# Kernel optimization log

Measured on AMD Instinct MI355X. Metric: run time of the kernel, lower is better.

## Reference

```python
import jax, jax.numpy as jnp
import numpy as np

N_PER_G = 6            # EEG channels per graph (complete graph incl. self-loops)
ALPHA = 0.5
BETA1 = float(np.log(1.0 / 1 + 1.0))  # GCN2Conv layer=1, lambda=1
BETA2 = float(np.log(1.0 / 2 + 1.0))  # GCN2Conv layer=2
BN_EPS = 1e-5


def setup_inputs() -> dict:
    key = jax.random.key(0)
    ks = jax.random.split(key, 10)
    G = 400_000
    N = G * N_PER_G          # 2.4M nodes
    E = G * N_PER_G * N_PER_G  # 14.4M edges (complete graph per EEG window)

    x = jax.random.normal(ks[0], (N, 6), dtype=jnp.float32)
    edge_weights = jax.random.uniform(ks[1], (E,), dtype=jnp.float32)

    # Batched complete-graph connectivity (numpy, structured)
    base = (np.arange(G, dtype=np.int64) * N_PER_G)
    ls = np.repeat(np.arange(N_PER_G), N_PER_G)   # local src
    ld = np.tile(np.arange(N_PER_G), N_PER_G)     # local dst
    src = jnp.asarray((base[:, None] + ls[None, :]).reshape(-1).astype(np.int32))
    dst = jnp.asarray((base[:, None] + ld[None, :]).reshape(-1).astype(np.int32))

    s6 = 1.0 / np.sqrt(6.0)
    W1 = jax.random.normal(ks[2], (6, 6), dtype=jnp.float32) * s6
    b1 = jnp.zeros((6,), dtype=jnp.float32)
    W2 = jax.random.normal(ks[3], (6, 6), dtype=jnp.float32) * s6
    b2 = jnp.zeros((6,), dtype=jnp.float32)
    gamma = jnp.ones((6,), dtype=jnp.float32)
    beta_bn = jnp.zeros((6,), dtype=jnp.float32)
    fcW1 = jax.random.normal(ks[4], (6, 10), dtype=jnp.float32) * s6   # xavier-ish
    fcb1 = jnp.zeros((10,), dtype=jnp.float32)
    fcW2 = jax.random.normal(ks[5], (10, 2), dtype=jnp.float32) * (1.0 / np.sqrt(10.0))
    fcb2 = jnp.zeros((2,), dtype=jnp.float32)

    return {"x": x, "edge_weights": edge_weights, "W1": W1, "b1": b1,
            "W2": W2, "b2": b2, "gamma": gamma, "beta_bn": beta_bn,
            "fcW1": fcW1, "fcb1": fcb1, "fcW2": fcW2, "fcb2": fcb2,
            "src": src, "dst": dst, "num_graphs": G}


def _gcn2_conv(feat, feat0, W, b, beta, edge_weights, src, dst, norm, n_nodes):
    # DGL GCN2Conv: sym-norm edge-weighted aggregation, identity mixing, proj mixing
    h = feat * norm                                   # [N,6]
    msg = h[src] * edge_weights[:, None]              # [E,6] gather
    agg = jax.ops.segment_sum(msg, dst, num_segments=n_nodes)  # [N,6] scatter-add
    h = agg * norm
    h = (1.0 - ALPHA) * h + ALPHA * feat0
    return (1.0 - beta) * h + beta * (h @ W) + b


def reference(x, edge_weights, W1, b1, W2, b2, gamma, beta_bn,
              fcW1, fcb1, fcW2, fcb2, src, dst, num_graphs):
    N = x.shape[0]
    # symmetric normalization from in-degrees (clamped to 1)
    deg = jax.ops.segment_sum(jnp.ones_like(edge_weights), dst, num_segments=N)
    norm = jax.lax.rsqrt(jnp.maximum(deg, 1.0))[:, None]  # [N,1]

    h = jax.nn.leaky_relu(_gcn2_conv(x, x, W1, b1, BETA1, edge_weights, src, dst, norm, N))
    h = _gcn2_conv(h, h, W2, b2, BETA2, edge_weights, src, dst, norm, N)

    # BatchNorm1d over nodes (training-mode batch statistics)
    mean = jnp.mean(h, axis=0)
    var = jnp.mean(jnp.square(h - mean), axis=0)
    h = (h - mean) * jax.lax.rsqrt(var + BN_EPS) * gamma + beta_bn
    h = jax.nn.leaky_relu(h)

    # SumPooling per graph (node i belongs to graph i // 6)
    gid = jnp.arange(N, dtype=jnp.int32) // N_PER_G
    pooled = jax.ops.segment_sum(h, gid, num_segments=num_graphs)  # [G,6]

    out = jax.nn.leaky_relu(pooled @ fcW1 + fcb1)  # dropout is identity at inference
    out = out @ fcW2 + fcb2                        # [G,2]
    return out
```

## Files before the change

### kernel.cpp

```cpp
#include <hip/hip_runtime.h>
#include <cstddef>
#include <cstdint>

#define NSLOT 64
#define ALPHA 0.5f
#define B1f   0.6931471805599453f
#define B2f   0.4054651081081644f

__device__ __forceinline__ float lrelu(float v) { return v >= 0.0f ? v : 0.01f * v; }

__device__ __forceinline__ float gc(const float4* a, int idx) {
  const float4 v = a[idx >> 2];
  const int c = idx & 3;
  return c == 0 ? v.x : (c == 1 ? v.y : (c == 2 ? v.z : v.w));
}

__device__ __forceinline__ unsigned pkbf(float a, float b) {
  unsigned ua = __float_as_uint(a), ub = __float_as_uint(b);
  ua += 0x7FFFu + ((ua >> 16) & 1u);
  ub += 0x7FFFu + ((ub >> 16) & 1u);
  return (ua >> 16) | (ub & 0xFFFF0000u);
}

__device__ __forceinline__ void gl_lds16(const float4* gp, float4* lbase, int lane) {
#if __has_builtin(__builtin_amdgcn_global_load_lds)
  __builtin_amdgcn_global_load_lds(
      (const __attribute__((address_space(1))) void*)(const void*)gp,
      (__attribute__((address_space(3))) void*)(void*)lbase, 16, 0, 0);
#else
  lbase[lane] = *gp;
#endif
}

__device__ __forceinline__ void compute_h2(const float4* X, const float4* Wt,
                                           const float* __restrict__ gW1,
                                           const float* __restrict__ gb1,
                                           const float* __restrict__ gW2,
                                           const float* __restrict__ gb2,
                                           float h2[36]) {
  float t[36];
#pragma unroll
  for (int j = 0; j < 6; ++j)
#pragma unroll
    for (int f = 0; f < 6; ++f) {
      float a = 0.f;
#pragma unroll
      for (int i = 0; i < 6; ++i) a = fmaf(gc(Wt, i * 6 + j), gc(X, i * 6 + f), a);
      t[j * 6 + f] = fmaf(a, ALPHA * (1.f / 6.f), ALPHA * gc(X, j * 6 + f));
    }
  float h1[36];
#pragma unroll
  for (int j = 0; j < 6; ++j)
#pragma unroll
    for (int f = 0; f < 6; ++f) {
      float a = 0.f;
#pragma unroll
      for (int k = 0; k < 6; ++k) a = fmaf(t[j * 6 + k], gW1[k * 6 + f], a);
      h1[j * 6 + f] = lrelu(fmaf(B1f, a, fmaf(1.f - B1f, t[j * 6 + f], gb1[f])));
    }
#pragma unroll
  for (int j = 0; j < 6; ++j)
#pragma unroll
    for (int f = 0; f < 6; ++f) {
      float a = 0.f;
#pragma unroll
      for (int i = 0; i < 6; ++i) a = fmaf(gc(Wt, i * 6 + j), h1[i * 6 + f], a);
      t[j * 6 + f] = fmaf(a, ALPHA * (1.f / 6.f), ALPHA * h1[j * 6 + f]);
    }
#pragma unroll
  for (int j = 0; j < 6; ++j)
#pragma unroll
    for (int f = 0; f < 6; ++f) {
      float a = 0.f;
#pragma unroll
      for (int k = 0; k < 6; ++k) a = fmaf(t[j * 6 + k], gW2[k * 6 + f], a);
      h2[j * 6 + f] = fmaf(B2f, a, fmaf(1.f - B2f, t[j * 6 + f], gb2[f]));
    }
}

__device__ __forceinline__ void bn_coeffs(const float* __restrict__ wsred,
                                          const float* __restrict__ gGamma,
                                          const float* __restrict__ gBeta,
                                          float invN, int lane,
                                          float sc[6], float sh[6]) {
  float st[12];
  const float4* p = reinterpret_cast<const float4*>(wsred) + (size_t)lane * 3;
  float4 a = p[0], b = p[1], c4 = p[2];
  st[0] = a.x;  st[1] = a.y;  st[2]  = a.z;  st[3]  = a.w;
  st[4] = b.x;  st[5] = b.y;  st[6]  = b.z;  st[7]  = b.w;
  st[8] = c4.x; st[9] = c4.y; st[10] = c4.z; st[11] = c4.w;
#pragma unroll
  for (int k = 0; k < 12; ++k)
#pragma unroll
    for (int o = 32; o >= 1; o >>= 1) st[k] += __shfl_xor(st[k], (unsigned)o, 64);
#pragma unroll
  for (int f = 0; f < 6; ++f) {
    float mean = st[f] * invN;
    float var  = st[6 + f] * invN - mean * mean;
    float s    = rsqrtf(var + 1e-5f) * gGamma[f];
    sc[f] = s;
    sh[f] = gBeta[f] - mean * s;
  }
}

__device__ __forceinline__ void pool_fc_out(const float h2[36],
                                            const float sc[6], const float sh[6],
                                            const float* __restrict__ fcW1,
                                            const float* __restrict__ fcb1,
                                            const float* __restrict__ fcW2,
                                            const float* __restrict__ fcb2,
                                            float2* __restrict__ out, int g) {
  float pooled[6] = {0.f, 0.f, 0.f, 0.f, 0.f, 0.f};
#pragma unroll
  for (int j = 0; j < 6; ++j)
#pragma unroll
    for (int f = 0; f < 6; ++f)
      pooled[f] += lrelu(fmaf(h2[j * 6 + f], sc[f], sh[f]));
  float p1[10];
#pragma unroll
  for (int m = 0; m < 10; ++m) {
    float a = fcb1[m];
#pragma unroll
    for (int f = 0; f < 6; ++f) a = fmaf(pooled[f], fcW1[f * 10 + m], a);
    p1[m] = lrelu(a);
  }
  float o0 = fcb2[0], o1 = fcb2[1];
#pragma unroll
  for (int m = 0; m < 10; ++m) {
    o0 = fmaf(p1[m], fcW2[m * 2 + 0], o0);
    o1 = fmaf(p1[m], fcW2[m * 2 + 1], o1);
  }
  out[g] = make_float2(o0, o1);
}

__global__ __launch_bounds__(256, 1) void gcn2_pass1(
    const float* __restrict__ x, const float* __restrict__ ew,
    const float* __restrict__ gW1, const float* __restrict__ gb1,
    const float* __restrict__ gW2, const float* __restrict__ gb2,
    float* __restrict__ wsred, unsigned* __restrict__ h2ws,
    int G, int useWs) {
  __shared__ float4 sbuf[4][2][1152];

  const int tid  = threadIdx.x;
  const int lane = tid & 63;
  const int wid  = tid >> 6;
  const int wgid = blockIdx.x * 4 + wid;
  const int wstr = gridDim.x * 4;
  const int nch  = (G + 63) >> 6;

  const float4* x4 = reinterpret_cast<const float4*>(x);
  const float4* w4 = reinterpret_cast<const float4*>(ew);
  const long fmax4 = (long)G * 9 - 1;

  float s[6]  = {0.f, 0.f, 0.f, 0.f, 0.f, 0.f};
  float ss[6] = {0.f, 0.f, 0.f, 0.f, 0.f, 0.f};

  int c = wgid;
  if (c < nch) {
    int cur = 0;
    {
#pragma unroll
      for (int k = 0; k < 9; ++k) {
        long fi = (long)c * 576 + k * 64 + lane;
        if (fi > fmax4) fi = fmax4;
        gl_lds16(x4 + fi, &sbuf[wid][0][k * 64], lane);
      }
#pragma unroll
      for (int k = 0; k < 9; ++k) {
        long fi = (long)c * 576 + k * 64 + lane;
        if (fi > fmax4) fi = fmax4;
        gl_lds16(w4 + fi, &sbuf[wid][0][576 + k * 64], lane);
      }
    }
    for (;;) {
      const int cn = c + wstr;
      const bool hn = cn < nch;
      if (hn) {
#pragma unroll
        for (int k = 0; k < 9; ++k) {
          long fi = (long)cn * 576 + k * 64 + lane;
          if (fi > fmax4) fi = fmax4;
          gl_lds16(x4 + fi, &sbuf[wid][cur ^ 1][k * 64], lane);
        }
#pragma unroll
        for (int k = 0; k < 9; ++k) {
          long fi = (long)cn * 576 + k * 64 + lane;
          if (fi > fmax4) fi = fmax4;
          gl_lds16(w4 + fi, &sbuf[wid][cur ^ 1][576 + k * 64], lane);
        }
      }
      __builtin_amdgcn_sched_barrier(0);
      if (hn) { __asm__ volatile("s_waitcnt vmcnt(18)" ::: "memory"); }
      else    { __asm__ volatile("s_waitcnt vmcnt(0)"  ::: "memory"); }
      __builtin_amdgcn_sched_barrier(0);

      {
        const float4* bx = &sbuf[wid][cur][lane * 9];
        const float4* bw = &sbuf[wid][cur][576 + lane * 9];
        float h2[36];
        compute_h2(bx, bw, gW1, gb1, gW2, gb2, h2);
        const int g = c * 64 + lane;
        if (g < G) {
          if (useWs) {
#pragma unroll
            for (int d = 0; d < 18; ++d)
              h2ws[(size_t)d * G + g] = pkbf(h2[2 * d], h2[2 * d + 1]);
          }
#pragma unroll
          for (int f = 0; f < 6; ++f)
#pragma unroll
            for (int j = 0; j < 6; ++j) {
              float v = h2[j * 6 + f];
              s[f] += v;
              ss[f] = fmaf(v, v, ss[f]);
            }
        }
      }
      if (!hn) break;
      __asm__ volatile("s_waitcnt lgkmcnt(0)" ::: "memory");
      __builtin_amdgcn_sched_barrier(0);
      c = cn;
      cur ^= 1;
    }
  }

#pragma unroll
  for (int f = 0; f < 6; ++f)
#pragma unroll
    for (int o = 32; o >= 1; o >>= 1) {
      s[f]  += __shfl_down(s[f],  (unsigned)o, 64);
      ss[f] += __shfl_down(ss[f], (unsigned)o, 64);
    }
  if (lane == 0) {
    float* p = wsred + (size_t)(wgid & (NSLOT - 1)) * 12;
#pragma unroll
    for (int f = 0; f < 6; ++f) {
      atomicAdd(p + f,     s[f]);
      atomicAdd(p + 6 + f, ss[f]);
    }
  }
}

__global__ __launch_bounds__(256) void gcn2_pass2ws(
    const unsigned* __restrict__ h2ws,
    const float* __restrict__ fcW1, const float* __restrict__ fcb1,
    const float* __restrict__ fcW2, const float* __restrict__ fcb2,
    const float* __restrict__ gGamma, const float* __restrict__ gBeta,
    const float* __restrict__ wsred, float invN,
    float2* __restrict__ out, int G) {
  const int tid  = threadIdx.x;
  const int lane = tid & 63;
  const int g    = blockIdx.x * 256 + tid;

  float sc[6], sh[6];
  bn_coeffs(wsred, gGamma, gBeta, invN, lane, sc, sh);

  if (g >= G) return;

  unsigned u[18];
#pragma unroll
  for (int d = 0; d < 18; ++d) u[d] = h2ws[(size_t)d * G + g];
  float h2[36];
#pragma unroll
  for (int d = 0; d < 18; ++d) {
    h2[2 * d]     = __uint_as_float(u[d] << 16);
    h2[2 * d + 1] = __uint_as_float(u[d] & 0xFFFF0000u);
  }
  pool_fc_out(h2, sc, sh, fcW1, fcb1, fcW2, fcb2, out, g);
}

__global__ __launch_bounds__(256) void gcn2_pass2re(
    const float* __restrict__ x, const float* __restrict__ ew,
    const float* __restrict__ gW1, const float* __restrict__ gb1,
    const float* __restrict__ gW2, const float* __restrict__ gb2,
    const float* __restrict__ fcW1, const float* __restrict__ fcb1,
    const float* __restrict__ fcW2, const float* __restrict__ fcb2,
    const float* __restrict__ gGamma, const float* __restrict__ gBeta,
    const float* __restrict__ wsred, float invN,
    float2* __restrict__ out, int G) {
  const int tid  = threadIdx.x;
  const int lane = tid & 63;
  const int g    = blockIdx.x * 256 + tid;

  float sc[6], sh[6];
  bn_coeffs(wsred, gGamma, gBeta, invN, lane, sc, sh);

  if (g >= G) return;

  const float4* px = reinterpret_cast<const float4*>(x)  + (size_t)g * 9;
  const float4* pw = reinterpret_cast<const float4*>(ew) + (size_t)g * 9;
  float4 X[9], Wv[9];
#pragma unroll
  for (int k = 0; k < 9; ++k) X[k]  = px[k];
#pragma unroll
  for (int k = 0; k < 9; ++k) Wv[k] = pw[k];
  float h2[36];
  compute_h2(X, Wv, gW1, gb1, gW2, gb2, h2);
  pool_fc_out(h2, sc, sh, fcW1, fcb1, fcW2, fcb2, out, g);
}

extern "C" void kernel_launch(void* const* d_in, const int* in_sizes, int n_in,
                              void* d_out, int out_size, void* d_ws, size_t ws_size,
                              hipStream_t stream) {
  const float* x     = (const float*)d_in[0];
  const float* ew    = (const float*)d_in[1];
  const float* W1    = (const float*)d_in[2];
  const float* b1    = (const float*)d_in[3];
  const float* W2    = (const float*)d_in[4];
  const float* b2    = (const float*)d_in[5];
  const float* gamma = (const float*)d_in[6];
  const float* beta  = (const float*)d_in[7];
  const float* fcW1  = (const float*)d_in[8];
  const float* fcb1  = (const float*)d_in[9];
  const float* fcW2  = (const float*)d_in[10];
  const float* fcb2  = (const float*)d_in[11];

  const int G = in_sizes[0] / 36;
  const float invN = 1.0f / (6.0f * (float)G);

  float*    wsred = (float*)d_ws;
  unsigned* h2ws  = (unsigned*)((char*)d_ws + 4096);
  const int useWs = (ws_size >= 4096 + (size_t)G * 72) ? 1 : 0;

  hipMemsetAsync(d_ws, 0, NSLOT * 12 * sizeof(float), stream);

  gcn2_pass1<<<256, 256, 0, stream>>>(x, ew, W1, b1, W2, b2,
                                      wsred, h2ws, G, useWs);
  const int grid2 = (G + 255) / 256;
  if (useWs) {
    gcn2_pass2ws<<<grid2, 256, 0, stream>>>(h2ws, fcW1, fcb1, fcW2, fcb2,
                                            gamma, beta, wsred, invN,
                                            (float2*)d_out, G);
  } else {
    gcn2_pass2re<<<grid2, 256, 0, stream>>>(x, ew, W1, b1, W2, b2,
                                            fcW1, fcb1, fcW2, fcb2,
                                            gamma, beta, wsred, invN,
                                            (float2*)d_out, G);
  }
}
```

Baseline: 48.06 us.

## Halve per-wave chunk size, double occupancy, and vectorize workspace layout

Each wave now processes 32 graphs per chunk instead of 64, which halves the LDS staging buffer so two blocks can be resident per CU, and the pass-1 grid is doubled to match. The bf16 workspace moves from 18 strided planes to four uint4 planes plus one uint2 plane, so both passes write and read it with wide vector accesses. The cost is that half the lanes sit idle during compute, because only lanes below 32 do work while all 64 lanes still issue the prefetch loads.

```diff
diff --git a/kernel.cpp b/kernel.cpp
--- a/kernel.cpp
+++ b/kernel.cpp
@@ -22,13 +22,13 @@
   return (ua >> 16) | (ub & 0xFFFF0000u);
 }
 
-__device__ __forceinline__ void gl_lds16(const float4* gp, float4* lbase, int lane) {
+__device__ __forceinline__ void gl_lds16(const float4* gp, float4* lbase) {
 #if __has_builtin(__builtin_amdgcn_global_load_lds)
   __builtin_amdgcn_global_load_lds(
       (const __attribute__((address_space(1))) void*)(const void*)gp,
       (__attribute__((address_space(3))) void*)(void*)lbase, 16, 0, 0);
 #else
-  lbase[lane] = *gp;
+  ((float4*)lbase)[threadIdx.x & 63] = *gp;
 #endif
 }
 
@@ -133,44 +133,40 @@
   out[g] = make_float2(o0, o1);
 }
 
-__global__ __launch_bounds__(256, 1) void gcn2_pass1(
+__global__ __launch_bounds__(256, 2) void gcn2_pass1(
     const float* __restrict__ x, const float* __restrict__ ew,
     const float* __restrict__ gW1, const float* __restrict__ gb1,
     const float* __restrict__ gW2, const float* __restrict__ gb2,
     float* __restrict__ wsred, unsigned* __restrict__ h2ws,
     int G, int useWs) {
-  __shared__ float4 sbuf[4][2][1152];
+  __shared__ float4 sbuf[4][2][576];
 
   const int tid  = threadIdx.x;
   const int lane = tid & 63;
   const int wid  = tid >> 6;
   const int wgid = blockIdx.x * 4 + wid;
   const int wstr = gridDim.x * 4;
-  const int nch  = (G + 63) >> 6;
+  const int nch  = (G + 31) >> 5;
 
   const float4* x4 = reinterpret_cast<const float4*>(x);
   const float4* w4 = reinterpret_cast<const float4*>(ew);
   const long fmax4 = (long)G * 9 - 1;
 
+  uint4* wsA = reinterpret_cast<uint4*>(h2ws);
+  uint2* wsB = reinterpret_cast<uint2*>(h2ws + (size_t)16 * G);
+
   float s[6]  = {0.f, 0.f, 0.f, 0.f, 0.f, 0.f};
   float ss[6] = {0.f, 0.f, 0.f, 0.f, 0.f, 0.f};
 
   int c = wgid;
   if (c < nch) {
     int cur = 0;
-    {
-#pragma unroll
-      for (int k = 0; k < 9; ++k) {
-        long fi = (long)c * 576 + k * 64 + lane;
-        if (fi > fmax4) fi = fmax4;
-        gl_lds16(x4 + fi, &sbuf[wid][0][k * 64], lane);
-      }
-#pragma unroll
-      for (int k = 0; k < 9; ++k) {
-        long fi = (long)c * 576 + k * 64 + lane;
-        if (fi > fmax4) fi = fmax4;
-        gl_lds16(w4 + fi, &sbuf[wid][0][576 + k * 64], lane);
-      }
+#pragma unroll
+    for (int k = 0; k < 9; ++k) {
+      const int F = k * 64 + lane;
+      long fi = (F < 288) ? ((long)c * 288 + F) : ((long)c * 288 + F - 288);
+      if (fi > fmax4) fi = fmax4;
+      gl_lds16(((F < 288) ? x4 : w4) + fi, &sbuf[wid][0][k * 64]);
     }
     for (;;) {
       const int cn = c + wstr;
@@ -178,33 +174,33 @@
       if (hn) {
 #pragma unroll
         for (int k = 0; k < 9; ++k) {
-          long fi = (long)cn * 576 + k * 64 + lane;
+          const int F = k * 64 + lane;
+          long fi = (F < 288) ? ((long)cn * 288 + F) : ((long)cn * 288 + F - 288);
           if (fi > fmax4) fi = fmax4;
-          gl_lds16(x4 + fi, &sbuf[wid][cur ^ 1][k * 64], lane);
-        }
-#pragma unroll
-        for (int k = 0; k < 9; ++k) {
-          long fi = (long)cn * 576 + k * 64 + lane;
-          if (fi > fmax4) fi = fmax4;
-          gl_lds16(w4 + fi, &sbuf[wid][cur ^ 1][576 + k * 64], lane);
+          gl_lds16(((F < 288) ? x4 : w4) + fi, &sbuf[wid][cur ^ 1][k * 64]);
         }
       }
       __builtin_amdgcn_sched_barrier(0);
-      if (hn) { __asm__ volatile("s_waitcnt vmcnt(18)" ::: "memory"); }
-      else    { __asm__ volatile("s_waitcnt vmcnt(0)"  ::: "memory"); }
+      if (hn) { __asm__ volatile("s_waitcnt vmcnt(9)" ::: "memory"); }
+      else    { __asm__ volatile("s_waitcnt vmcnt(0)" ::: "memory"); }
       __builtin_amdgcn_sched_barrier(0);
 
-      {
-        const float4* bx = &sbuf[wid][cur][lane * 9];
-        const float4* bw = &sbuf[wid][cur][576 + lane * 9];
-        float h2[36];
-        compute_h2(bx, bw, gW1, gb1, gW2, gb2, h2);
-        const int g = c * 64 + lane;
+      if (lane < 32) {
+        const int g = c * 32 + lane;
         if (g < G) {
+          const float4* bx = &sbuf[wid][cur][lane * 9];
+          const float4* bw = &sbuf[wid][cur][288 + lane * 9];
+          float h2[36];
+          compute_h2(bx, bw, gW1, gb1, gW2, gb2, h2);
           if (useWs) {
-#pragma unroll
-            for (int d = 0; d < 18; ++d)
-              h2ws[(size_t)d * G + g] = pkbf(h2[2 * d], h2[2 * d + 1]);
+            unsigned d[18];
+#pragma unroll
+            for (int k = 0; k < 18; ++k) d[k] = pkbf(h2[2 * k], h2[2 * k + 1]);
+            wsA[(size_t)0 * G + g] = make_uint4(d[0],  d[1],  d[2],  d[3]);
+            wsA[(size_t)1 * G + g] = make_uint4(d[4],  d[5],  d[6],  d[7]);
+            wsA[(size_t)2 * G + g] = make_uint4(d[8],  d[9],  d[10], d[11]);
+            wsA[(size_t)3 * G + g] = make_uint4(d[12], d[13], d[14], d[15]);
+            wsB[g]                 = make_uint2(d[16], d[17]);
           }
 #pragma unroll
           for (int f = 0; f < 6; ++f)
@@ -257,9 +253,21 @@
 
   if (g >= G) return;
 
+  const uint4* wsA = reinterpret_cast<const uint4*>(h2ws);
+  const uint2* wsB = reinterpret_cast<const uint2*>(h2ws + (size_t)16 * G);
   unsigned u[18];
-#pragma unroll
-  for (int d = 0; d < 18; ++d) u[d] = h2ws[(size_t)d * G + g];
+  {
+    uint4 a0 = wsA[(size_t)0 * G + g];
+    uint4 a1 = wsA[(size_t)1 * G + g];
+    uint4 a2 = wsA[(size_t)2 * G + g];
+    uint4 a3 = wsA[(size_t)3 * G + g];
+    uint2 b0 = wsB[g];
+    u[0]=a0.x; u[1]=a0.y; u[2]=a0.z;  u[3]=a0.w;
+    u[4]=a1.x; u[5]=a1.y; u[6]=a1.z;  u[7]=a1.w;
+    u[8]=a2.x; u[9]=a2.y; u[10]=a2.z; u[11]=a2.w;
+    u[12]=a3.x; u[13]=a3.y; u[14]=a3.z; u[15]=a3.w;
+    u[16]=b0.x; u[17]=b0.y;
+  }
   float h2[36];
 #pragma unroll
   for (int d = 0; d < 18; ++d) {
@@ -324,7 +332,7 @@
 
   hipMemsetAsync(d_ws, 0, NSLOT * 12 * sizeof(float), stream);
 
-  gcn2_pass1<<<256, 256, 0, stream>>>(x, ew, W1, b1, W2, b2,
+  gcn2_pass1<<<512, 256, 0, stream>>>(x, ew, W1, b1, W2, b2,
                                       wsred, h2ws, G, useWs);
   const int grid2 = (G + 255) / 256;
   if (useWs) {
```

New measurement: 55.33 us. 1.15x slower.
